# Performance work log

Measured on AMD Instinct MI355X. Metric: run time of the kernel, lower is better.

Reference implementation:

```python
import jax, jax.numpy as jnp
import numpy as np

DIM = 1024
L = 10
C = 1.0
SQRT_C = float(np.sqrt(C))


def _exp_map(x, v, c):
    # Poincare exp map (general form, as in the torch source)
    xn2 = jnp.sum(x * x, axis=-1, keepdims=True)
    lam = 2.0 / (1.0 - c * xn2)
    vn = jnp.sqrt(jnp.sum(v * v, axis=-1, keepdims=True))
    vn = jnp.maximum(vn, 1e-8)
    second = jnp.tanh(SQRT_C * lam * vn / 2.0) / (SQRT_C * vn) * v
    num = (1.0 - c * xn2) * second
    den = (1.0 - 2.0 * c * jnp.sum(x * second, axis=-1, keepdims=True)
           + c * c * xn2 * jnp.sum(second * second, axis=-1, keepdims=True))
    return x + num / den


def _log_map(x, y, c):
    # Poincare log map (general form, as in the torch source)
    xn2 = jnp.sum(x * x, axis=-1, keepdims=True)
    lam = 2.0 / (1.0 - c * xn2)
    yn2 = jnp.sum(y * y, axis=-1, keepdims=True)
    xy = jnp.sum(x * y, axis=-1, keepdims=True)
    tv = (-x * yn2 + y * (1.0 + c * xn2) - 2.0 * c * xy * x) / (1.0 - c * xn2)
    tn = jnp.sqrt(jnp.sum(tv * tv, axis=-1, keepdims=True))
    num = 2.0 * SQRT_C * jnp.arctanh(SQRT_C * tn)
    den = SQRT_C * lam * tn
    return num / den * tv


def _butterfly(u, params):
    # Stage l: blocks of size 2^l along the feature dim; within each block,
    # adjacent pairs are rotated by that block's (a, b) Givens-like rotation.
    # Param layout matches __init__: for layer l there are dim>>l blocks,
    # 2 params (a, b) each, laid out contiguously layer after layer.
    B = u.shape[0]
    offset = 0
    for l in range(L):
        bs = 1 << l
        nb = DIM // bs
        seg = params[offset:offset + 2 * nb]
        offset += 2 * nb
        if bs < 2:
            continue  # block of size 1 has no pair to rotate
        ab = seg.reshape(nb, 2)
        a = ab[:, 0][None, :, None]  # [1, nb, 1]
        b = ab[:, 1][None, :, None]
        u4 = u.reshape(B, nb, bs // 2, 2)
        u0 = u4[..., 0]
        u1 = u4[..., 1]
        u = jnp.stack([a * u0 + b * u1, -b * u0 + a * u1], axis=-1).reshape(B, DIM)
    return u


def setup_inputs() -> dict:
    key = jax.random.key(0)
    k1, k2 = jax.random.split(key)
    # points inside the Poincare ball: per-row norm ~ 0.01*sqrt(1024) ~ 0.32
    x = jax.random.normal(k1, (32768, DIM), dtype=jnp.float32) * 0.01
    P = 2 * sum(DIM >> l for l in range(L))  # 4092
    base = jnp.tile(jnp.array([0.9, 0.0], dtype=jnp.float32), P // 2)
    params = base + 0.1 * jax.random.normal(k2, (P,), dtype=jnp.float32)
    return {"x": x, "params": params}


def reference(x, params):
    u = _log_map(jnp.zeros_like(x), x, C)
    u = _butterfly(u, params)
    return _exp_map(jnp.zeros_like(u), u, C)
```

## Files before the change

kernel.cpp:

```cpp
#include <hip/hip_runtime.h>
#include <math.h>

#define DIM 1024
#define NPAIRS 512

typedef float f32x4 __attribute__((ext_vector_type(4)));

__global__ __launch_bounds__(256) void hyper_butterfly_fused_kernel(
        const float* __restrict__ x,
        const float* __restrict__ params,
        float* __restrict__ out,
        int rows) {
    const int lane = threadIdx.x & 63;
    const int wave = threadIdx.x >> 6;
    const int row = blockIdx.x * 4 + wave;
    if (row >= rows) return;

    const float4* xrow = (const float4*)(x + (size_t)row * DIM);
    float4 xv[4];
#pragma unroll
    for (int i = 0; i < 4; ++i) xv[i] = xrow[lane + 64 * i];

    const float2* pf2 = (const float2*)params;
    float4 wv[4];
#pragma unroll
    for (int i = 0; i < 4; ++i) {
        const int q = lane + 64 * i;
        float cr = 1.0f, ci = 0.0f;
        const int F[8] = {1536, 1792, 1920, 1984, 2016, 2032, 2040, 2044};
#pragma unroll
        for (int l = 0; l < 8; ++l) {
            float2 ab = pf2[F[l] + (q >> l)];
            float nr = cr * ab.x + ci * ab.y;
            float ni = ci * ab.x - cr * ab.y;
            cr = nr;
            ci = ni;
        }
        float2 ab0 = pf2[1024 + 2 * q];
        float2 ab1 = pf2[1024 + 2 * q + 1];
        wv[i].x = cr * ab0.x + ci * ab0.y;
        wv[i].y = ci * ab0.x - cr * ab0.y;
        wv[i].z = cr * ab1.x + ci * ab1.y;
        wv[i].w = ci * ab1.x - cr * ab1.y;
    }

    float p1 = 0.0f, p2 = 0.0f;
#pragma unroll
    for (int i = 0; i < 4; ++i) {
        float a0 = xv[i].x * xv[i].x + xv[i].y * xv[i].y;
        float a1 = xv[i].z * xv[i].z + xv[i].w * xv[i].w;
        float m0 = wv[i].x * wv[i].x + wv[i].y * wv[i].y;
        float m1 = wv[i].z * wv[i].z + wv[i].w * wv[i].w;
        p1 += a0 + a1;
        p2 += m0 * a0 + m1 * a1;
    }

#pragma unroll
    for (int o = 32; o > 0; o >>= 1) {
        p1 += __shfl_xor(p1, o);
        p2 += __shfl_xor(p2, o);
    }

    float r = sqrtf(p1);
    float s1 = (r > 1e-12f) ? (0.5f * logf((1.0f + r) / (1.0f - r)) / r)
                            : 1.0f;
    float vn = fmaxf(s1 * sqrtf(p2), 1e-8f);
    float s = s1 * (tanhf(vn) / vn);

    f32x4* orow = (f32x4*)(out + (size_t)row * DIM);
#pragma unroll
    for (int i = 0; i < 4; ++i) {
        f32x4 o4;
        o4.x = s * (wv[i].x * xv[i].x - wv[i].y * xv[i].y);
        o4.y = s * (wv[i].x * xv[i].y + wv[i].y * xv[i].x);
        o4.z = s * (wv[i].z * xv[i].z - wv[i].w * xv[i].w);
        o4.w = s * (wv[i].z * xv[i].w + wv[i].w * xv[i].z);
        __builtin_nontemporal_store(o4, &orow[lane + 64 * i]);
    }
}

extern "C" void kernel_launch(void* const* d_in, const int* in_sizes, int n_in,
                              void* d_out, int out_size, void* d_ws, size_t ws_size,
                              hipStream_t stream) {
    const float* x = (const float*)d_in[0];
    const float* params = (const float*)d_in[1];
    float* out = (float*)d_out;

    int rows = in_sizes[0] / DIM;

    int blocks = (rows + 3) / 4;
    hyper_butterfly_fused_kernel<<<blocks, 256, 0, stream>>>(
        x, params, out, rows);
}
```

Before: 233.8 us.

## Split fused kernel into separate row-reduction and scaling kernels

Replaces the single fused kernel with two launches. The first reads x, computes per-row norms using only the squared magnitude of the composed rotation coefficients, and writes one scale per row to workspace, or into the output buffer if workspace is too small. The second re-reads x and the scale, recomputes the complex coefficients, and writes the scaled output. This removes the reduction and transcendental work from the store path, but reads x from memory twice and adds a launch.

```diff
diff --git a/kernel.cpp b/kernel.cpp
--- a/kernel.cpp
+++ b/kernel.cpp
@@ -2,13 +2,69 @@
 #include <math.h>
 
 #define DIM 1024
-#define NPAIRS 512
 
 typedef float f32x4 __attribute__((ext_vector_type(4)));
 
-__global__ __launch_bounds__(256) void hyper_butterfly_fused_kernel(
+
+#define F_TABLE {1536, 1792, 1920, 1984, 2016, 2032, 2040, 2044}
+
+__global__ __launch_bounds__(256) void hb_reduce_kernel(
         const float* __restrict__ x,
         const float* __restrict__ params,
+        float* __restrict__ srow, int sstride,
+        int rows) {
+    const int lane = threadIdx.x & 63;
+    const int wave = threadIdx.x >> 6;
+    const int row = blockIdx.x * 4 + wave;
+    if (row >= rows) return;
+
+    const float4* xrow = (const float4*)(x + (size_t)row * DIM);
+    float4 xv[4];
+#pragma unroll
+    for (int i = 0; i < 4; ++i) xv[i] = xrow[lane + 64 * i];
+
+    const float2* pf2 = (const float2*)params;
+    float p1 = 0.0f, p2 = 0.0f;
+#pragma unroll
+    for (int i = 0; i < 4; ++i) {
+        const int q = lane + 64 * i;
+        const int F[8] = F_TABLE;
+        float c2 = 1.0f;
+#pragma unroll
+        for (int l = 0; l < 8; ++l) {
+            float2 ab = pf2[F[l] + (q >> l)];
+            c2 *= ab.x * ab.x + ab.y * ab.y;
+        }
+        float2 ab0 = pf2[1024 + 2 * q];
+        float2 ab1 = pf2[1024 + 2 * q + 1];
+        float m0 = c2 * (ab0.x * ab0.x + ab0.y * ab0.y);
+        float m1 = c2 * (ab1.x * ab1.x + ab1.y * ab1.y);
+        float a0 = xv[i].x * xv[i].x + xv[i].y * xv[i].y;
+        float a1 = xv[i].z * xv[i].z + xv[i].w * xv[i].w;
+        p1 += a0 + a1;
+        p2 += m0 * a0 + m1 * a1;
+    }
+
+#pragma unroll
+    for (int o = 32; o > 0; o >>= 1) {
+        p1 += __shfl_xor(p1, o);
+        p2 += __shfl_xor(p2, o);
+    }
+
+    if (lane == 0) {
+        float r = sqrtf(p1);
+        float s1 = (r > 1e-12f)
+                       ? (0.5f * logf((1.0f + r) / (1.0f - r)) / r)
+                       : 1.0f;
+        float vn = fmaxf(s1 * sqrtf(p2), 1e-8f);
+        srow[(size_t)row * sstride] = s1 * (tanhf(vn) / vn);
+    }
+}
+
+__global__ __launch_bounds__(256) void hb_scale_kernel(
+        const float* __restrict__ x,
+        const float* __restrict__ params,
+        const float* __restrict__ srow, int sstride,
         float* __restrict__ out,
         int rows) {
     const int lane = threadIdx.x & 63;
@@ -21,13 +77,15 @@
 #pragma unroll
     for (int i = 0; i < 4; ++i) xv[i] = xrow[lane + 64 * i];
 
+    float s = srow[(size_t)row * sstride];
+
     const float2* pf2 = (const float2*)params;
     float4 wv[4];
 #pragma unroll
     for (int i = 0; i < 4; ++i) {
         const int q = lane + 64 * i;
+        const int F[8] = F_TABLE;
         float cr = 1.0f, ci = 0.0f;
-        const int F[8] = {1536, 1792, 1920, 1984, 2016, 2032, 2040, 2044};
 #pragma unroll
         for (int l = 0; l < 8; ++l) {
             float2 ab = pf2[F[l] + (q >> l)];
@@ -43,29 +101,6 @@
         wv[i].z = cr * ab1.x + ci * ab1.y;
         wv[i].w = ci * ab1.x - cr * ab1.y;
     }
-
-    float p1 = 0.0f, p2 = 0.0f;
-#pragma unroll
-    for (int i = 0; i < 4; ++i) {
-        float a0 = xv[i].x * xv[i].x + xv[i].y * xv[i].y;
-        float a1 = xv[i].z * xv[i].z + xv[i].w * xv[i].w;
-        float m0 = wv[i].x * wv[i].x + wv[i].y * wv[i].y;
-        float m1 = wv[i].z * wv[i].z + wv[i].w * wv[i].w;
-        p1 += a0 + a1;
-        p2 += m0 * a0 + m1 * a1;
-    }
-
-#pragma unroll
-    for (int o = 32; o > 0; o >>= 1) {
-        p1 += __shfl_xor(p1, o);
-        p2 += __shfl_xor(p2, o);
-    }
-
-    float r = sqrtf(p1);
-    float s1 = (r > 1e-12f) ? (0.5f * logf((1.0f + r) / (1.0f - r)) / r)
-                            : 1.0f;
-    float vn = fmaxf(s1 * sqrtf(p2), 1e-8f);
-    float s = s1 * (tanhf(vn) / vn);
 
     f32x4* orow = (f32x4*)(out + (size_t)row * DIM);
 #pragma unroll
@@ -88,7 +123,17 @@
 
     int rows = in_sizes[0] / DIM;
 
+    float* srow;
+    int sstride;
+    if (ws_size >= (size_t)rows * sizeof(float)) {
+        srow = (float*)d_ws;
+        sstride = 1;
+    } else {
+        srow = out;
+        sstride = DIM;
+    }
+
     int blocks = (rows + 3) / 4;
-    hyper_butterfly_fused_kernel<<<blocks, 256, 0, stream>>>(
-        x, params, out, rows);
+    hb_reduce_kernel<<<blocks, 256, 0, stream>>>(x, params, srow, sstride, rows);
+    hb_scale_kernel<<<blocks, 256, 0, stream>>>(x, params, srow, sstride, out, rows);
 }
```

After: 252.2 us. 1.08x slower.

## Use persistent waves with double-buffered row prefetch and hoisted butterfly weights

Applied to the files above, without the earlier changes.

Switches to a persistent grid capped at 1024 blocks, so each wave computes the collapsed butterfly weights and their squared magnitudes once and then processes many rows in a grid-stride loop. The next row is loaded into a second register buffer while the current row is reduced and stored, to overlap memory latency with compute. This removes the per-row cost of recomputing weights from params, but raises register pressure and lowers the number of resident waves available to hide latency.

```diff
diff --git a/kernel.cpp b/kernel.cpp
--- a/kernel.cpp
+++ b/kernel.cpp
@@ -2,65 +2,34 @@
 #include <math.h>
 
 #define DIM 1024
-#define NPAIRS 512
 
 typedef float f32x4 __attribute__((ext_vector_type(4)));
 
-__global__ __launch_bounds__(256) void hyper_butterfly_fused_kernel(
-        const float* __restrict__ x,
-        const float* __restrict__ params,
-        float* __restrict__ out,
-        int rows) {
-    const int lane = threadIdx.x & 63;
-    const int wave = threadIdx.x >> 6;
-    const int row = blockIdx.x * 4 + wave;
-    if (row >= rows) return;
 
+__device__ __forceinline__ void hb_load_row(const float* __restrict__ x,
+                                            int row, int lane, float4 v[4]) {
     const float4* xrow = (const float4*)(x + (size_t)row * DIM);
-    float4 xv[4];
 #pragma unroll
-    for (int i = 0; i < 4; ++i) xv[i] = xrow[lane + 64 * i];
+    for (int i = 0; i < 4; ++i) v[i] = xrow[lane + 64 * i];
+}
 
-    const float2* pf2 = (const float2*)params;
-    float4 wv[4];
-#pragma unroll
-    for (int i = 0; i < 4; ++i) {
-        const int q = lane + 64 * i;
-        float cr = 1.0f, ci = 0.0f;
-        const int F[8] = {1536, 1792, 1920, 1984, 2016, 2032, 2040, 2044};
-#pragma unroll
-        for (int l = 0; l < 8; ++l) {
-            float2 ab = pf2[F[l] + (q >> l)];
-            float nr = cr * ab.x + ci * ab.y;
-            float ni = ci * ab.x - cr * ab.y;
-            cr = nr;
-            ci = ni;
-        }
-        float2 ab0 = pf2[1024 + 2 * q];
-        float2 ab1 = pf2[1024 + 2 * q + 1];
-        wv[i].x = cr * ab0.x + ci * ab0.y;
-        wv[i].y = ci * ab0.x - cr * ab0.y;
-        wv[i].z = cr * ab1.x + ci * ab1.y;
-        wv[i].w = ci * ab1.x - cr * ab1.y;
-    }
-
+__device__ __forceinline__ void hb_process_store(
+        const float4 xv[4], const float4 wv[4],
+        const float m0[4], const float m1[4],
+        float* __restrict__ out, int row, int lane) {
     float p1 = 0.0f, p2 = 0.0f;
 #pragma unroll
     for (int i = 0; i < 4; ++i) {
         float a0 = xv[i].x * xv[i].x + xv[i].y * xv[i].y;
         float a1 = xv[i].z * xv[i].z + xv[i].w * xv[i].w;
-        float m0 = wv[i].x * wv[i].x + wv[i].y * wv[i].y;
-        float m1 = wv[i].z * wv[i].z + wv[i].w * wv[i].w;
         p1 += a0 + a1;
-        p2 += m0 * a0 + m1 * a1;
+        p2 += m0[i] * a0 + m1[i] * a1;
     }
-
 #pragma unroll
     for (int o = 32; o > 0; o >>= 1) {
         p1 += __shfl_xor(p1, o);
         p2 += __shfl_xor(p2, o);
     }
-
     float r = sqrtf(p1);
     float s1 = (r > 1e-12f) ? (0.5f * logf((1.0f + r) / (1.0f - r)) / r)
                             : 1.0f;
@@ -79,6 +48,60 @@
     }
 }
 
+__global__ __launch_bounds__(256) void hb_persistent_kernel(
+        const float* __restrict__ x,
+        const float* __restrict__ params,
+        float* __restrict__ out,
+        int rows) {
+    const int lane = threadIdx.x & 63;
+    const int gwave = blockIdx.x * 4 + (threadIdx.x >> 6);
+    const int nwaves = gridDim.x * 4;
+
+    int rowA = gwave;
+    if (rowA >= rows) return;
+
+    float4 A[4], B[4];
+    hb_load_row(x, rowA, lane, A);
+
+    const float2* pf2 = (const float2*)params;
+    float4 wv[4];
+    float m0[4], m1[4];
+#pragma unroll
+    for (int i = 0; i < 4; ++i) {
+        const int q = lane + 64 * i;
+        const int F[8] = {1536, 1792, 1920, 1984, 2016, 2032, 2040, 2044};
+        float cr = 1.0f, ci = 0.0f;
+#pragma unroll
+        for (int l = 0; l < 8; ++l) {
+            float2 ab = pf2[F[l] + (q >> l)];
+            float nr = cr * ab.x + ci * ab.y;
+            float ni = ci * ab.x - cr * ab.y;
+            cr = nr;
+            ci = ni;
+        }
+        float2 ab0 = pf2[1024 + 2 * q];
+        float2 ab1 = pf2[1024 + 2 * q + 1];
+        wv[i].x = cr * ab0.x + ci * ab0.y;
+        wv[i].y = ci * ab0.x - cr * ab0.y;
+        wv[i].z = cr * ab1.x + ci * ab1.y;
+        wv[i].w = ci * ab1.x - cr * ab1.y;
+        m0[i] = wv[i].x * wv[i].x + wv[i].y * wv[i].y;
+        m1[i] = wv[i].z * wv[i].z + wv[i].w * wv[i].w;
+    }
+
+    for (;;) {
+        int rowB = rowA + nwaves;
+        if (rowB < rows) hb_load_row(x, rowB, lane, B);
+        hb_process_store(A, wv, m0, m1, out, rowA, lane);
+        if (rowB >= rows) return;
+
+        rowA = rowB + nwaves;
+        if (rowA < rows) hb_load_row(x, rowA, lane, A);
+        hb_process_store(B, wv, m0, m1, out, rowB, lane);
+        if (rowA >= rows) return;
+    }
+}
+
 extern "C" void kernel_launch(void* const* d_in, const int* in_sizes, int n_in,
                               void* d_out, int out_size, void* d_ws, size_t ws_size,
                               hipStream_t stream) {
@@ -88,7 +111,8 @@
 
     int rows = in_sizes[0] / DIM;
 
-    int blocks = (rows + 3) / 4;
-    hyper_butterfly_fused_kernel<<<blocks, 256, 0, stream>>>(
-        x, params, out, rows);
+    int maxb = 1024;
+    int need = (rows + 3) / 4;
+    int blocks = need < maxb ? need : maxb;
+    hb_persistent_kernel<<<blocks, 256, 0, stream>>>(x, params, out, rows);
 }
```

Result: no change. 235.2 us (+0.6%).
